# Performance work log

Hardware: AMD Instinct MI355X
Metric: run time of the kernel (lower is better)

## Reference

```python
import jax, jax.numpy as jnp
import numpy as np

B, T, C_IN = 2, 4096, 1024
INTER, OUT = 1024, 1024
ROPE_DIM = 64
GAMMA = 0.99609375  # 1 - 2**-8
GROUPS = 32
EPS = 1e-6


def setup_inputs() -> dict:
    key = jax.random.key(0)
    k = jax.random.split(key, 4)
    return {
        "X_Q": jax.random.normal(k[0], (B, T, C_IN), dtype=jnp.float32),
        "W_Q": jax.random.normal(k[1], (C_IN, INTER), dtype=jnp.float32) / C_IN,
        "W_K": jax.random.normal(k[2], (C_IN, INTER), dtype=jnp.float32) / C_IN,
        "W_V": jax.random.normal(k[3], (C_IN, OUT), dtype=jnp.float32) / C_IN,
        "gn_weight": jnp.ones((OUT,), dtype=jnp.float32),
        "gn_bias": jnp.zeros((OUT,), dtype=jnp.float32),
    }


def _rope(x):
    # lucidrains RotaryEmbedding: rotate first ROPE_DIM features, pairwise-adjacent
    t = x.shape[-2]
    inv_freq = 1.0 / (10000.0 ** (jnp.arange(0, ROPE_DIM, 2, dtype=jnp.float32) / ROPE_DIM))
    freqs = jnp.arange(t, dtype=jnp.float32)[:, None] * inv_freq[None, :]  # [T, ROPE_DIM/2]
    freqs = jnp.repeat(freqs, 2, axis=-1)                                   # [T, ROPE_DIM]
    cos, sin = jnp.cos(freqs), jnp.sin(freqs)
    xr, xp = x[..., :ROPE_DIM], x[..., ROPE_DIM:]
    x1, x2 = xr[..., 0::2], xr[..., 1::2]
    rot = jnp.stack([-x2, x1], axis=-1).reshape(xr.shape)  # rotate_half (adjacent pairs)
    return jnp.concatenate([xr * cos + rot * sin, xp], axis=-1)


def _group_norm(x, w, b):
    # torch GroupNorm applied on x.reshape(-1, C)
    sh = x.shape
    c = sh[-1]
    xr = x.reshape(-1, GROUPS, c // GROUPS)
    mu = xr.mean(-1, keepdims=True)
    var = xr.var(-1, keepdims=True)
    xn = ((xr - mu) * jax.lax.rsqrt(var + EPS)).reshape(-1, c)
    return (xn * w + b).reshape(sh)


def reference(X_Q, W_Q, W_K, W_V, gn_weight, gn_bias):
    Q = jax.nn.silu(_rope(X_Q @ W_Q))  # [B,T,INTER]
    K = jax.nn.silu(_rope(X_Q @ W_K))
    V = jax.nn.silu(X_Q @ W_V)         # [B,T,OUT]
    A = jnp.einsum('btd,bsd->bts', Q, K)  # [B,T,T]
    # decay mask: original multiplies by _get_D(gamma,T).T -> gamma^(m-n) for m>=n
    n = jnp.arange(T)[:, None]
    m = jnp.arange(T)[None, :]
    upper = m >= n
    Dt = jnp.where(upper, GAMMA ** jnp.where(upper, m - n, 0).astype(jnp.float32), 0.0)
    A = A * Dt
    out = jnp.einsum('bts,bsd->btd', A, V)  # [B,T,OUT]
    # dropout p=0 (eval) -> identity
    return _group_norm(out, gn_weight, gn_bias)
```

## Files before the change

kernel.cpp:

```cpp
#include <hip/hip_runtime.h>


typedef __attribute__((ext_vector_type(8))) short bf16x8;
typedef __attribute__((ext_vector_type(4))) short bf16x4;
typedef __attribute__((ext_vector_type(4))) float f32x4;

#define MFMA16(a, b, c) __builtin_amdgcn_mfma_f32_16x16x32_bf16(a, b, c, 0, 0, 0)

static __device__ __forceinline__ short f2bf(float f) {
  unsigned u = __builtin_bit_cast(unsigned, f);
  u = (u + 0x7fffu + ((u >> 16) & 1u)) >> 16;
  return (short)u;
}

static __device__ __forceinline__ float fast_silu(float v) {
  return v * __builtin_amdgcn_rcpf(1.f + __expf(-v));
}

static __device__ __forceinline__ void gl_lds16(const void* g, void* l) {
  __builtin_amdgcn_global_load_lds(
      (const __attribute__((address_space(1))) void*)g,
      (__attribute__((address_space(3))) void*)l, 16, 0, 0);
}

static __device__ __forceinline__ int swzc(int col, int row) {
  return (((col >> 3) ^ (row & 7)) << 3) | (col & 7);
}

#define T_LEN 4096
#define CIN 1024

#define LOG2G (-0.0056465633f)
#define L2IF (0.41524101f)

__global__ __launch_bounds__(256)
void prep_kernel(const float* __restrict__ X, short* __restrict__ Xb,
                 const float* __restrict__ Wq, const float* __restrict__ Wk,
                 const float* __restrict__ Wv, short* __restrict__ WT) {
  __shared__ short tile[64][72];
  const int bx = blockIdx.x;
  const int tid = threadIdx.x;
  if (bx < 4096) {
    const int gid = bx * 256 + tid;
    const int row = gid >> 7;
    const int c = gid & 127;
    const float* s = &X[(size_t)gid * 8];
    float4 f0 = *(const float4*)s;
    float4 f1 = *(const float4*)(s + 4);
    bf16x8 v = {f2bf(f0.x), f2bf(f0.y), f2bf(f0.z), f2bf(f0.w),
                f2bf(f1.x), f2bf(f1.y), f2bf(f1.z), f2bf(f1.w)};
    const int pc = (c & 0x78) | ((c ^ row) & 7);
    *(bf16x8*)&Xb[(size_t)row * 1024 + pc * 8] = v;
    return;
  }
  const int bx2 = bx - 4096;
  const int k0 = (bx2 & 15) * 64, n0 = ((bx2 >> 4) & 15) * 64, mat = bx2 >> 8;
  const float* __restrict__ W = (mat == 0) ? Wq : (mat == 1) ? Wk : Wv;
  const int r = tid >> 4, c = tid & 15;
#pragma unroll
  for (int i = 0; i < 4; ++i) {
    int row = r + 16 * i;
    float4 f = *(const float4*)&W[(size_t)(k0 + row) * CIN + n0 + c * 4];
    tile[c * 4 + 0][row] = f2bf(f.x);
    tile[c * 4 + 1][row] = f2bf(f.y);
    tile[c * 4 + 2][row] = f2bf(f.z);
    tile[c * 4 + 3][row] = f2bf(f.w);
  }
  __syncthreads();
  const int n = tid >> 2, seg = tid & 3;
  bf16x8 lo = *(const bf16x8*)&tile[n][seg * 16];
  bf16x8 hi = *(const bf16x8*)&tile[n][seg * 16 + 8];
  const int R = mat * 1024 + n0 + n;
  const int a0 = (k0 >> 3) + seg * 2;
  short* base = &WT[(size_t)R * CIN];
  *(bf16x8*)&base[(a0 ^ (n & 7)) * 8] = lo;
  *(bf16x8*)&base[((a0 + 1) ^ (n & 7)) * 8] = hi;
}

#define GEMM_DECLS()                                   \
  const int tid = threadIdx.x;                         \
  const int lane = tid & 63, wave = tid >> 6;          \
  const int wm = wave >> 1, wn = wave & 1;             \
  const int l15 = lane & 15, quad = lane >> 4;         \
  const int srow = tid >> 3;                           \
  const int scol = (tid & 7) * 8;                      \
  const int asw = (l15 & 7);

#define ACC_INIT4(acc)                                 \
  _Pragma("unroll") for (int i = 0; i < 4; ++i)        \
  _Pragma("unroll") for (int j = 0; j < 4; ++j) {      \
    f32x4 z = {0.f, 0.f, 0.f, 0.f};                    \
    acc[i][j] = z;                                     \
  }

#define STAGE_TILE(dst, src, ld, r0, k0, nrows)        \
  _Pragma("unroll") for (int i = 0; i < (nrows) / 32; ++i) \
    gl_lds16(&src[(size_t)((r0) + i * 32 + srow) * (ld) + (k0) + scol], \
             &dst[i * 32 + srow][scol]);

#define FRAG_MFMA44(As, Bs, acc)                                            \
  {                                                                         \
    bf16x8 af[4][2], bfr[4][2];                                             \
    _Pragma("unroll") for (int im = 0; im < 4; ++im)                        \
    _Pragma("unroll") for (int ks = 0; ks < 2; ++ks)                        \
      af[im][ks] = *(const bf16x8*)&As[wm * 64 + im * 16 + l15]             \
                       [((ks * 4 + quad) ^ asw) * 8];                       \
    _Pragma("unroll") for (int in = 0; in < 4; ++in)                        \
    _Pragma("unroll") for (int ks = 0; ks < 2; ++ks)                        \
      bfr[in][ks] = *(const bf16x8*)&Bs[wn * 64 + in * 16 + l15]            \
                        [((ks * 4 + quad) ^ asw) * 8];                      \
    _Pragma("unroll") for (int ks = 0; ks < 2; ++ks)                        \
    _Pragma("unroll") for (int im = 0; im < 4; ++im)                        \
    _Pragma("unroll") for (int in = 0; in < 4; ++in)                        \
      acc[im][in] = MFMA16(af[im][ks], bfr[in][ks], acc[im][in]);           \
  }

__global__ __launch_bounds__(256, 2)
void qkv_gemm(const short* __restrict__ Xb, const short* __restrict__ WT,
              short* __restrict__ Qb, short* __restrict__ Kb,
              short* __restrict__ Vt) {
  __shared__ __align__(16) short As[128][64];
  __shared__ __align__(16) short Bs[128][64];
  GEMM_DECLS();
  const int m0 = blockIdx.x * 128;
  const int c0 = blockIdx.y * 128;

  f32x4 acc[4][4];
  ACC_INIT4(acc);

  for (int k0 = 0; k0 < CIN; k0 += 64) {
    __syncthreads();
    STAGE_TILE(As, Xb, CIN, m0, k0, 128);
    STAGE_TILE(Bs, WT, CIN, c0, k0, 128);
    __syncthreads();
    FRAG_MFMA44(As, Bs, acc);
  }

  const int mat = (c0 >> 10);
  const bool ropeBlk = (mat < 2) && ((c0 & 1023) == 0);
#pragma unroll
  for (int im = 0; im < 4; ++im) {
#pragma unroll
    for (int in = 0; in < 4; ++in) {
      const int c = c0 + wn * 64 + in * 16 + l15;
      const int colm = c & 1023;
      const int mbase = m0 + wm * 64 + im * 16 + quad * 4;
      short vv[4];
      if (ropeBlk && colm < 64) {
        const float invf = exp2f(-L2IF * (float)(colm >> 1));
#pragma unroll
        for (int r = 0; r < 4; ++r) {
          float v = acc[im][in][r];
          int t = (mbase + r) & (T_LEN - 1);
          float partner = __shfl_xor(v, 1, 64);
          float ang = (float)t * invf;
          float s_ = __sinf(ang), c_ = __cosf(ang);
          v = (colm & 1) ? (v * c_ + partner * s_) : (v * c_ - partner * s_);
          vv[r] = f2bf(fast_silu(v));
        }
      } else {
#pragma unroll
        for (int r = 0; r < 4; ++r) vv[r] = f2bf(fast_silu(acc[im][in][r]));
      }
      if (mat == 0) {
#pragma unroll
        for (int r = 0; r < 4; ++r)
          Qb[(size_t)(mbase + r) * 1024 + swzc(colm, mbase + r)] = vv[r];
      } else if (mat == 1) {
#pragma unroll
        for (int r = 0; r < 4; ++r)
          Kb[(size_t)(mbase + r) * 1024 + swzc(colm, mbase + r)] = vv[r];
      } else {
        bf16x4 v4 = {vv[0], vv[1], vv[2], vv[3]};
        *(bf16x4*)&Vt[(size_t)colm * 8192 +
                      (((mbase >> 3) ^ (colm & 7)) << 3) + (mbase & 7)] = v4;
      }
    }
  }
}

__global__ __launch_bounds__(256, 2)
void score_kernel(const short* __restrict__ Qb, const short* __restrict__ Kb,
                  short* __restrict__ Ab) {
  int idx = blockIdx.x;
  int ti = 0;
  while (idx >= 32 - ti) { idx -= 32 - ti; ++ti; }
  const int si = ti + idx;
  const int b = blockIdx.y;
  const int s0 = si * 128, t0 = ti * 128;

  __shared__ __align__(16) short Qs[128][64];
  __shared__ __align__(16) short Ks[128][64];
  GEMM_DECLS();

  f32x4 acc[4][4];
  ACC_INIT4(acc);

  for (int k0 = 0; k0 < 1024; k0 += 64) {
    __syncthreads();
    STAGE_TILE(Qs, Qb, 1024, b * T_LEN + t0, k0, 128);
    STAGE_TILE(Ks, Kb, 1024, b * T_LEN + s0, k0, 128);
    __syncthreads();
    FRAG_MFMA44(Qs, Ks, acc);
  }

#pragma unroll
  for (int im = 0; im < 4; ++im) {
#pragma unroll
    for (int in = 0; in < 4; ++in) {
      int s = s0 + wn * 64 + in * 16 + l15;
#pragma unroll
      for (int r = 0; r < 4; ++r) {
        int t = t0 + wm * 64 + im * 16 + quad * 4 + r;
        int d = s - t;
        float v = acc[im][in][r];
        v = (d < 0) ? 0.f : v * exp2f((float)d * LOG2G);
        Ab[((size_t)(b * T_LEN + t)) * T_LEN + swzc(s, t)] = f2bf(v);
      }
    }
  }
}

__global__ __launch_bounds__(256, 2)
void av_kernel(const short* __restrict__ Ab, const short* __restrict__ Vt,
               const float* __restrict__ gw, const float* __restrict__ gb,
               float* __restrict__ Out) {
  const int p = blockIdx.x, b = blockIdx.y, di = blockIdx.z;
  const int n0 = di * 128;

  __shared__ __align__(16) short As2[64][64];
  __shared__ __align__(16) short Vs[128][64];
  GEMM_DECLS();

  float w4[4], b4[4];
#pragma unroll
  for (int in = 0; in < 4; ++in) {
    int n = n0 + wn * 64 + in * 16 + l15;
    w4[in] = gw[n];
    b4[in] = gb[n];
  }

#pragma unroll 1
  for (int half = 0; half < 2; ++half) {
    const int ti2 = half ? (63 - p) : p;
    const int t0 = ti2 * 64;

    f32x4 acc[2][4];
#pragma unroll
    for (int i = 0; i < 2; ++i)
#pragma unroll
      for (int j = 0; j < 4; ++j) {
        f32x4 z = {0.f, 0.f, 0.f, 0.f};
        acc[i][j] = z;
      }

    for (int s = t0; s < T_LEN; s += 64) {
      __syncthreads();
      STAGE_TILE(As2, Ab, T_LEN, b * T_LEN + t0, s, 64);
      STAGE_TILE(Vs, Vt, 8192, n0, b * T_LEN + s, 128);
      __syncthreads();
      bf16x8 af[2][2], bfr[4][2];
#pragma unroll
      for (int im = 0; im < 2; ++im)
#pragma unroll
        for (int ks = 0; ks < 2; ++ks)
          af[im][ks] = *(const bf16x8*)&As2[wm * 32 + im * 16 + l15]
                           [((ks * 4 + quad) ^ asw) * 8];
#pragma unroll
      for (int in = 0; in < 4; ++in)
#pragma unroll
        for (int ks = 0; ks < 2; ++ks)
          bfr[in][ks] = *(const bf16x8*)&Vs[wn * 64 + in * 16 + l15]
                            [((ks * 4 + quad) ^ asw) * 8];
#pragma unroll
      for (int ks = 0; ks < 2; ++ks)
#pragma unroll
        for (int im = 0; im < 2; ++im)
#pragma unroll
          for (int in = 0; in < 4; ++in)
            acc[im][in] = MFMA16(af[im][ks], bfr[in][ks], acc[im][in]);
    }

#pragma unroll
    for (int im = 0; im < 2; ++im) {
#pragma unroll
      for (int r = 0; r < 4; ++r) {
        int t = t0 + wm * 32 + im * 16 + quad * 4 + r;
        float* orow = &Out[((size_t)(b * T_LEN + t)) * 1024];
#pragma unroll
        for (int g = 0; g < 2; ++g) {
          float a0 = acc[im][g * 2][r], a1 = acc[im][g * 2 + 1][r];
          float s = a0 + a1;
          float q = a0 * a0 + a1 * a1;
          s += __shfl_xor(s, 1, 64);
          q += __shfl_xor(q, 1, 64);
          s += __shfl_xor(s, 2, 64);
          q += __shfl_xor(q, 2, 64);
          s += __shfl_xor(s, 4, 64);
          q += __shfl_xor(q, 4, 64);
          s += __shfl_xor(s, 8, 64);
          q += __shfl_xor(q, 8, 64);
          float mean = s * (1.f / 32.f);
          float var = q * (1.f / 32.f) - mean * mean;
          float rstd = rsqrtf(var + 1e-6f);
          int n = n0 + wn * 64 + g * 32 + l15;
          orow[n] = (a0 - mean) * rstd * w4[g * 2] + b4[g * 2];
          orow[n + 16] = (a1 - mean) * rstd * w4[g * 2 + 1] + b4[g * 2 + 1];
        }
      }
    }
  }
}

extern "C" void kernel_launch(void* const* d_in, const int* in_sizes, int n_in,
                              void* d_out, int out_size, void* d_ws,
                              size_t ws_size, hipStream_t stream) {
  const float* X = (const float*)d_in[0];
  const float* Wq = (const float*)d_in[1];
  const float* Wk = (const float*)d_in[2];
  const float* Wv = (const float*)d_in[3];
  const float* gw = (const float*)d_in[4];
  const float* gb = (const float*)d_in[5];
  float* Out = (float*)d_out;

  short* Qb = (short*)d_ws;
  short* Kb = Qb + (size_t)8192 * 1024;
  short* Vt = Kb + (size_t)8192 * 1024;
  short* Ab = Vt + (size_t)8192 * 1024;
  short* Xb = Ab;
  short* WT = Xb + (size_t)8192 * 1024;

  prep_kernel<<<4864, 256, 0, stream>>>(X, Xb, Wq, Wk, Wv, WT);
  qkv_gemm<<<dim3(64, 24), 256, 0, stream>>>(Xb, WT, Qb, Kb, Vt);
  score_kernel<<<dim3(528, 2), 256, 0, stream>>>(Qb, Kb, Ab);
  av_kernel<<<dim3(32, 2, 8), 256, 0, stream>>>(Ab, Vt, gw, gb, Out);
}
```

Before: 289.8 us.

## Enlarge av_kernel tile to 128 rows with a flat one-tile-per-block grid

Each av_kernel block now computes a single 128x128 output tile instead of two paired 64-row tiles. Each staged V tile is therefore reused across twice as many query rows, which cuts global and LDS traffic for V. Blocks use a flattened 512-block grid, and the two batches are mapped to mirrored tile orders to spread the triangular work. The cost is more accumulator registers per thread and less even work per block, since a block now runs anywhere from 2 to 64 iterations.

```diff
diff --git a/kernel.cpp b/kernel.cpp
--- a/kernel.cpp
+++ b/kernel.cpp
@@ -225,10 +225,17 @@
 void av_kernel(const short* __restrict__ Ab, const short* __restrict__ Vt,
                const float* __restrict__ gw, const float* __restrict__ gb,
                float* __restrict__ Out) {
-  const int p = blockIdx.x, b = blockIdx.y, di = blockIdx.z;
+  const int wgid = blockIdx.x;
+  const int di = wgid & 7;
+  const int q = (wgid >> 3) & 31;
+  const int half = wgid >> 8;
+  const int b = half;
+  const int ti2 = half ? (31 - q) : q;
+  const int t0 = ti2 * 128;
   const int n0 = di * 128;
-
-  __shared__ __align__(16) short As2[64][64];
+  const int nIt = (T_LEN - t0) >> 6;
+
+  __shared__ __align__(16) short As2[128][64];
   __shared__ __align__(16) short Vs[128][64];
   GEMM_DECLS();
 
@@ -240,73 +247,44 @@
     b4[in] = gb[n];
   }
 
+  f32x4 acc[4][4];
+  ACC_INIT4(acc);
+
 #pragma unroll 1
-  for (int half = 0; half < 2; ++half) {
-    const int ti2 = half ? (63 - p) : p;
-    const int t0 = ti2 * 64;
-
-    f32x4 acc[2][4];
-#pragma unroll
-    for (int i = 0; i < 2; ++i)
-#pragma unroll
-      for (int j = 0; j < 4; ++j) {
-        f32x4 z = {0.f, 0.f, 0.f, 0.f};
-        acc[i][j] = z;
-      }
-
-    for (int s = t0; s < T_LEN; s += 64) {
-      __syncthreads();
-      STAGE_TILE(As2, Ab, T_LEN, b * T_LEN + t0, s, 64);
-      STAGE_TILE(Vs, Vt, 8192, n0, b * T_LEN + s, 128);
-      __syncthreads();
-      bf16x8 af[2][2], bfr[4][2];
-#pragma unroll
-      for (int im = 0; im < 2; ++im)
-#pragma unroll
-        for (int ks = 0; ks < 2; ++ks)
-          af[im][ks] = *(const bf16x8*)&As2[wm * 32 + im * 16 + l15]
-                           [((ks * 4 + quad) ^ asw) * 8];
-#pragma unroll
-      for (int in = 0; in < 4; ++in)
-#pragma unroll
-        for (int ks = 0; ks < 2; ++ks)
-          bfr[in][ks] = *(const bf16x8*)&Vs[wn * 64 + in * 16 + l15]
-                            [((ks * 4 + quad) ^ asw) * 8];
-#pragma unroll
-      for (int ks = 0; ks < 2; ++ks)
-#pragma unroll
-        for (int im = 0; im < 2; ++im)
-#pragma unroll
-          for (int in = 0; in < 4; ++in)
-            acc[im][in] = MFMA16(af[im][ks], bfr[in][ks], acc[im][in]);
-    }
-
-#pragma unroll
-    for (int im = 0; im < 2; ++im) {
-#pragma unroll
-      for (int r = 0; r < 4; ++r) {
-        int t = t0 + wm * 32 + im * 16 + quad * 4 + r;
-        float* orow = &Out[((size_t)(b * T_LEN + t)) * 1024];
-#pragma unroll
-        for (int g = 0; g < 2; ++g) {
-          float a0 = acc[im][g * 2][r], a1 = acc[im][g * 2 + 1][r];
-          float s = a0 + a1;
-          float q = a0 * a0 + a1 * a1;
-          s += __shfl_xor(s, 1, 64);
-          q += __shfl_xor(q, 1, 64);
-          s += __shfl_xor(s, 2, 64);
-          q += __shfl_xor(q, 2, 64);
-          s += __shfl_xor(s, 4, 64);
-          q += __shfl_xor(q, 4, 64);
-          s += __shfl_xor(s, 8, 64);
-          q += __shfl_xor(q, 8, 64);
-          float mean = s * (1.f / 32.f);
-          float var = q * (1.f / 32.f) - mean * mean;
-          float rstd = rsqrtf(var + 1e-6f);
-          int n = n0 + wn * 64 + g * 32 + l15;
-          orow[n] = (a0 - mean) * rstd * w4[g * 2] + b4[g * 2];
-          orow[n + 16] = (a1 - mean) * rstd * w4[g * 2 + 1] + b4[g * 2 + 1];
-        }
+  for (int it = 0; it < nIt; ++it) {
+    const int s = t0 + (it << 6);
+    __syncthreads();
+    STAGE_TILE(As2, Ab, T_LEN, b * T_LEN + t0, s, 128);
+    STAGE_TILE(Vs, Vt, 8192, n0, b * T_LEN + s, 128);
+    __syncthreads();
+    FRAG_MFMA44(As2, Vs, acc);
+  }
+
+#pragma unroll
+  for (int im = 0; im < 4; ++im) {
+#pragma unroll
+    for (int r = 0; r < 4; ++r) {
+      int t = t0 + wm * 64 + im * 16 + quad * 4 + r;
+      float* orow = &Out[((size_t)(b * T_LEN + t)) * 1024];
+#pragma unroll
+      for (int g = 0; g < 2; ++g) {
+        float a0 = acc[im][g * 2][r], a1 = acc[im][g * 2 + 1][r];
+        float s = a0 + a1;
+        float qq = a0 * a0 + a1 * a1;
+        s += __shfl_xor(s, 1, 64);
+        qq += __shfl_xor(qq, 1, 64);
+        s += __shfl_xor(s, 2, 64);
+        qq += __shfl_xor(qq, 2, 64);
+        s += __shfl_xor(s, 4, 64);
+        qq += __shfl_xor(qq, 4, 64);
+        s += __shfl_xor(s, 8, 64);
+        qq += __shfl_xor(qq, 8, 64);
+        float mean = s * (1.f / 32.f);
+        float var = qq * (1.f / 32.f) - mean * mean;
+        float rstd = rsqrtf(var + 1e-6f);
+        int n = n0 + wn * 64 + g * 32 + l15;
+        orow[n] = (a0 - mean) * rstd * w4[g * 2] + b4[g * 2];
+        orow[n + 16] = (a1 - mean) * rstd * w4[g * 2 + 1] + b4[g * 2 + 1];
       }
     }
   }
@@ -333,5 +311,5 @@
   prep_kernel<<<4864, 256, 0, stream>>>(X, Xb, Wq, Wk, Wv, WT);
   qkv_gemm<<<dim3(64, 24), 256, 0, stream>>>(Xb, WT, Qb, Kb, Vt);
   score_kernel<<<dim3(528, 2), 256, 0, stream>>>(Qb, Kb, Ab);
-  av_kernel<<<dim3(32, 2, 8), 256, 0, stream>>>(Ab, Vt, gw, gb, Out);
-}
+  av_kernel<<<512, 256, 0, stream>>>(Ab, Vt, gw, gb, Out);
+}
```

Measured after the change: 280.9 us. 1.03x faster.
